# Kernel tuning notes

Measured on AMD Instinct MI355X. Metric: run time of the kernel, lower is better.

## Reference

```python
import jax, jax.numpy as jnp
import numpy as np

EPS = 1e-10

def _pairwise_cos_dist(X, Y):
    # X: (N, c), Y: (M, c) -> (N, M) cosine distance, matching torch impl exactly
    x_norm = jnp.sqrt(jnp.sum(X * X, axis=1, keepdims=True))          # (N, 1)
    y_norm = jnp.sqrt(jnp.sum(Y * Y, axis=1, keepdims=True)).T        # (1, M)
    return 1.0 - (X @ Y.T) / (x_norm + EPS) / (y_norm + EPS)

def _style_loss_cos(X, Y):
    D = _pairwise_cos_dist(X, Y)
    m1 = jnp.min(D, axis=1).mean()  # relaxed EMD, row mins
    m2 = jnp.min(D, axis=0).mean()  # col mins
    return jnp.maximum(m1, m2)

def _moment_loss(X, Y):
    # X, Y: (N, c)
    n = X.shape[0]
    mu_x = X.mean(axis=0, keepdims=True)
    mu_y = Y.mean(axis=0, keepdims=True)
    mu_d = jnp.abs(mu_x - mu_y).mean()
    Xc = X - mu_x
    Yc = Y - mu_y
    X_cov = (Xc.T @ Xc) / (n - 1)   # (c, c)
    Y_cov = (Yc.T @ Yc) / (n - 1)
    return mu_d + jnp.abs(X_cov - Y_cov).mean()

def _level_loss(X, Y):
    # X, Y: (N, c) per-batch, per-level feature sets
    return _style_loss_cos(X, Y) + _moment_loss(X, Y)

_per_batch_level_loss = jax.vmap(_level_loss)  # over leading batch dim

def _gather_points(feat, idx):
    # feat: (B, c, h, w), idx: (B, N) spatial indices -> (B, N, c)
    B, c, h, w = feat.shape
    flat = feat.reshape(B, c, h * w)
    g = jnp.take_along_axis(flat, idx[:, None, :], axis=2)  # (B, c, N)
    return jnp.swapaxes(g, 1, 2)

def _all_points(feat):
    # feat: (B, c, h, w) -> (B, h*w, c); used when h <= 32 (no subsampling)
    B, c, h, w = feat.shape
    return jnp.swapaxes(feat.reshape(B, c, h * w), 1, 2)

def setup_inputs() -> dict:
    key = jax.random.key(0)
    ks = jax.random.split(key, 11)
    shapes = [(8, 64, 256, 256), (8, 128, 128, 128), (8, 256, 64, 64), (8, 512, 32, 32)]
    inp = {}
    for i, s in enumerate(shapes):
        inp[f"target_feat{i}"] = jax.random.normal(ks[i], s, dtype=jnp.float32)
        inp[f"gen_feat{i}"] = jax.random.normal(ks[4 + i], s, dtype=jnp.float32)
    for j, hw in enumerate([256 * 256, 128 * 128, 64 * 64]):
        inp[f"idx{j}"] = jnp.sort(
            jax.random.randint(ks[8 + j], (8, 1000), 0, hw, dtype=jnp.int32), axis=1
        )
    return inp

def reference(target_feat0, target_feat1, target_feat2, target_feat3,
              gen_feat0, gen_feat1, gen_feat2, gen_feat3,
              idx0, idx1, idx2):
    B = target_feat0.shape[0]
    loss_b = jnp.zeros((B,), dtype=target_feat0.dtype)
    # levels 0-2: h > 32 -> subsample 1000 spatial points
    for t, g, idx in [(target_feat0, gen_feat0, idx0),
                      (target_feat1, gen_feat1, idx1),
                      (target_feat2, gen_feat2, idx2)]:
        loss_b = loss_b + _per_batch_level_loss(_gather_points(t, idx), _gather_points(g, idx))
    # level 3: h == 32 -> use all 1024 points
    loss_b = loss_b + _per_batch_level_loss(_all_points(target_feat3), _all_points(gen_feat3))
    return loss_b.mean()  # sum over batch / batch_size
```

## Files before the change

kernel.cpp:

```cpp
#include <hip/hip_runtime.h>
#include <cstdint>
#include <cstddef>

#define EPSC 1e-10f
typedef unsigned short u16;
typedef unsigned int u32;
typedef __attribute__((ext_vector_type(8))) short bf16x8;
typedef __attribute__((ext_vector_type(4))) float f32x4;

#define XTX_B 0u
#define XTY_B 7864320u
#define XNX_B 15728640u
#define XNY_B 23592960u
#define FB 15728640u
#define RNX_OFF (FB + 0u)
#define RNY_OFF (FB + 32768u)
#define RMIN_OFF (FB + 65536u)
#define CMIN_OFF (FB + 98304u)
#define MUX_OFF (FB + 131072u)
#define MUY_OFF (FB + 138752u)
#define COVS_OFF (FB + 146432u)
#define ACC_OFF (FB + 146464u)

struct Tabs { int c[4], N[4], mo[4]; u32 off[4]; };

__device__ __forceinline__ u16 f2bf(float f) {
  u32 u = __float_as_uint(f);
  u = (u + 0x7fffu + ((u >> 16) & 1u)) >> 16;
  return (u16)u;
}
__device__ __forceinline__ float bf2f(u16 h) { return __uint_as_float(((u32)h) << 16); }

__global__ void k_init(float* __restrict__ wsf) {
  int i = blockIdx.x * blockDim.x + threadIdx.x;
  if (i < 65536) ((unsigned*)(wsf + RMIN_OFF))[i] = 0x7f800000u;
  if (i < 33) wsf[COVS_OFF + i] = 0.f;
}

__global__ void k_gather(const float* __restrict__ tsrc, const float* __restrict__ gsrc,
                         const int* __restrict__ idx,
                         u16* __restrict__ xt, u16* __restrict__ yt,
                         u16* __restrict__ xn, u16* __restrict__ yn,
                         int c, int hw, int N) {
  __shared__ float Ls[64 * 67];
  int z = blockIdx.z, which = z >> 3, b = z & 7;
  int c0 = blockIdx.y * 64, n0 = blockIdx.x * 64;
  int tid = threadIdx.x;
  const float* src = which ? gsrc : tsrc;
  u16* dt = (which ? yt : xt) + (size_t)b * c * 1024;
  u16* dn = (which ? yn : xn) + (size_t)b * c * 1024;
  int nl = tid & 63, cb = tid >> 6;
  int n = n0 + nl;
  bool nv = n < N;
  int sp = nv ? (idx ? idx[b * N + n] : n) : 0;
  const float* sbase = src + ((size_t)b * c + c0) * hw;
#pragma unroll
  for (int r = 0; r < 16; ++r) {
    int ch = cb + r * 4;
    Ls[ch * 67 + nl] = nv ? sbase[(size_t)ch * hw + sp] : 0.f;
  }
  __syncthreads();
#pragma unroll
  for (int r = 0; r < 16; ++r) {
    int ch = cb + r * 4;
    dt[(size_t)(c0 + ch) * 1024 + n] = f2bf(Ls[ch * 67 + nl]);
  }
#pragma unroll
  for (int r = 0; r < 16; ++r) {
    int nw = cb + r * 4;
    int chw = nl;
    dn[(size_t)(n0 + nw) * c + c0 + chw] = f2bf(Ls[chw * 67 + nw]);
  }
}

__global__ void k_rnorm(const u16* __restrict__ bfb, float* __restrict__ wsf, Tabs t) {
  int L = blockIdx.z;
  int c = t.c[L];
  int zy = blockIdx.y, which = zy >> 3, b = zy & 7;
  int n = blockIdx.x * 256 + threadIdx.x;
  const u16* P = bfb + (which ? XTY_B : XTX_B) + t.off[L] + (size_t)b * c * 1024;
  float s = 0.f;
  for (int ch = 0; ch < c; ch += 4) {
#pragma unroll
    for (int u = 0; u < 4; ++u) {
      float v = bf2f(P[(size_t)(ch + u) * 1024 + n]);
      s = fmaf(v, v, s);
    }
  }
  int z = L * 8 + b;
  wsf[(which ? RNY_OFF : RNX_OFF) + (size_t)z * 1024 + n] = 1.0f / (sqrtf(s) + EPSC);
}

__global__ void k_mu(const u16* __restrict__ bfb, float* __restrict__ wsf, Tabs t) {
  int L = blockIdx.z;
  int c = t.c[L], N = t.N[L];
  int zy = blockIdx.y, which = zy >> 3, b = zy & 7;
  int wv = threadIdx.x >> 6, lane = threadIdx.x & 63;
  int ch = blockIdx.x * 4 + wv;
  if (ch >= c) return;
  const u16* P = bfb + (which ? XTY_B : XTX_B) + t.off[L] + ((size_t)b * c + ch) * 1024;
  float s = 0.f;
  for (int n = lane; n < 1024; n += 64) s += bf2f(P[n]);
#pragma unroll
  for (int off = 32; off; off >>= 1) s += __shfl_down(s, off, 64);
  if (lane == 0) wsf[(which ? MUY_OFF : MUX_OFF) + t.mo[L] + (size_t)b * c + ch] = s * (1.0f / N);
}

__global__ __launch_bounds__(256) void k_cosmin(const u16* __restrict__ bfb, float* __restrict__ wsf, Tabs t) {
  __shared__ __align__(16) u16 As[128 * 72];
  __shared__ __align__(16) u16 Bs[128 * 72];
  int z = blockIdx.z, L = z >> 3, b = z & 7;
  int c = t.c[L], N = t.N[L];
  const u16* X = bfb + XNX_B + t.off[L] + (size_t)b * c * 1024;
  const u16* Y = bfb + XNY_B + t.off[L] + (size_t)b * c * 1024;
  int i0 = blockIdx.x * 128, j0 = blockIdx.y * 128;
  int tid = threadIdx.x, lane = tid & 63, w = tid >> 6;
  int wi = w >> 1, wj = w & 1, q = lane >> 4, cl = lane & 15;
  f32x4 acc[4][4] = {};
  int srow = tid >> 3, sch = tid & 7;
  for (int k0 = 0; k0 < c; k0 += 64) {
#pragma unroll
    for (int rep = 0; rep < 4; ++rep) {
      int row = srow + rep * 32;
      uint4 va = *(const uint4*)(X + (size_t)(i0 + row) * c + k0 + sch * 8);
      uint4 vb = *(const uint4*)(Y + (size_t)(j0 + row) * c + k0 + sch * 8);
      *(uint4*)(As + row * 72 + sch * 8) = va;
      *(uint4*)(Bs + row * 72 + sch * 8) = vb;
    }
    __syncthreads();
#pragma unroll
    for (int h = 0; h < 2; ++h) {
      bf16x8 af[4], bq[4];
#pragma unroll
      for (int ti = 0; ti < 4; ++ti)
        af[ti] = *(const bf16x8*)(As + (wi * 64 + ti * 16 + cl) * 72 + h * 32 + q * 8);
#pragma unroll
      for (int tj = 0; tj < 4; ++tj)
        bq[tj] = *(const bf16x8*)(Bs + (wj * 64 + tj * 16 + cl) * 72 + h * 32 + q * 8);
#pragma unroll
      for (int ti = 0; ti < 4; ++ti)
#pragma unroll
        for (int tj = 0; tj < 4; ++tj)
          acc[ti][tj] = __builtin_amdgcn_mfma_f32_16x16x32_bf16(af[ti], bq[tj], acc[ti][tj], 0, 0, 0);
    }
    __syncthreads();
  }
  const float* rnx = wsf + RNX_OFF + (size_t)z * 1024;
  const float* rny = wsf + RNY_OFF + (size_t)z * 1024;
  unsigned* rminp = (unsigned*)(wsf + RMIN_OFF) + (size_t)z * 1024;
  unsigned* cminp = (unsigned*)(wsf + CMIN_OFF) + (size_t)z * 1024;
  const float INFV = __uint_as_float(0x7f800000u);
  int colg[4]; float rnyv[4]; float colmin[4];
#pragma unroll
  for (int tj = 0; tj < 4; ++tj) {
    colg[tj] = j0 + wj * 64 + tj * 16 + cl;
    rnyv[tj] = rny[colg[tj]];
    colmin[tj] = INFV;
  }
#pragma unroll
  for (int ti = 0; ti < 4; ++ti) {
#pragma unroll
    for (int r = 0; r < 4; ++r) {
      int rowg = i0 + wi * 64 + ti * 16 + q * 4 + r;
      float rx = rnx[rowg];
      bool rv = rowg < N;
      float rmin = INFV;
#pragma unroll
      for (int tj = 0; tj < 4; ++tj) {
        float d = 1.0f - acc[ti][tj][r] * rx * rnyv[tj];
        if (!rv || colg[tj] >= N) d = INFV;
        rmin = fminf(rmin, d);
        colmin[tj] = fminf(colmin[tj], d);
      }
      rmin = fminf(rmin, __shfl_xor(rmin, 1, 64));
      rmin = fminf(rmin, __shfl_xor(rmin, 2, 64));
      rmin = fminf(rmin, __shfl_xor(rmin, 4, 64));
      rmin = fminf(rmin, __shfl_xor(rmin, 8, 64));
      if (cl == 0 && rv) atomicMin(&rminp[rowg], __float_as_uint(rmin));
    }
  }
#pragma unroll
  for (int tj = 0; tj < 4; ++tj) {
    float cm = colmin[tj];
    cm = fminf(cm, __shfl_xor(cm, 16, 64));
    cm = fminf(cm, __shfl_xor(cm, 32, 64));
    if (q == 0 && colg[tj] < N) atomicMin(&cminp[colg[tj]], __float_as_uint(cm));
  }
}

__global__ __launch_bounds__(256) void k_cov(const u16* __restrict__ bfb, float* __restrict__ wsf, Tabs t) {
  __shared__ __align__(16) u16 SXA[128 * 40], SXB[128 * 40], SYA[128 * 40], SYB[128 * 40];
  __shared__ float wsum[4];
  int z = blockIdx.z, L = z >> 3, b = z & 7;
  int c = t.c[L], N = t.N[L];
  int ca = (c + 127) >> 7;
  if ((int)blockIdx.x >= ca || (int)blockIdx.y >= ca) return;
  int a0 = blockIdx.x * 128, b0 = blockIdx.y * 128;
  const u16* XT = bfb + XTX_B + t.off[L] + (size_t)b * c * 1024;
  const u16* YT = bfb + XTY_B + t.off[L] + (size_t)b * c * 1024;
  int tid = threadIdx.x, lane = tid & 63, w = tid >> 6;
  int wi = w >> 1, wj = w & 1, q = lane >> 4, cl = lane & 15;
  f32x4 gx[4][4] = {}, gy[4][4] = {};
  int srow = tid >> 2, sch = tid & 3;
  for (int k0 = 0; k0 < 1024; k0 += 32) {
#pragma unroll
    for (int rep = 0; rep < 2; ++rep) {
      int rr = srow + rep * 64;
      int ra = a0 + rr, rb = b0 + rr;
      uint4 zz = make_uint4(0u, 0u, 0u, 0u);
      uint4 xa = (ra < c) ? *(const uint4*)(XT + (size_t)ra * 1024 + k0 + sch * 8) : zz;
      uint4 xb = (rb < c) ? *(const uint4*)(XT + (size_t)rb * 1024 + k0 + sch * 8) : zz;
      uint4 ya = (ra < c) ? *(const uint4*)(YT + (size_t)ra * 1024 + k0 + sch * 8) : zz;
      uint4 yb = (rb < c) ? *(const uint4*)(YT + (size_t)rb * 1024 + k0 + sch * 8) : zz;
      *(uint4*)(SXA + rr * 40 + sch * 8) = xa;
      *(uint4*)(SXB + rr * 40 + sch * 8) = xb;
      *(uint4*)(SYA + rr * 40 + sch * 8) = ya;
      *(uint4*)(SYB + rr * 40 + sch * 8) = yb;
    }
    __syncthreads();
    bf16x8 af[4], bq[4];
#pragma unroll
    for (int ti = 0; ti < 4; ++ti) af[ti] = *(const bf16x8*)(SXA + (wi * 64 + ti * 16 + cl) * 40 + q * 8);
#pragma unroll
    for (int tj = 0; tj < 4; ++tj) bq[tj] = *(const bf16x8*)(SXB + (wj * 64 + tj * 16 + cl) * 40 + q * 8);
#pragma unroll
    for (int ti = 0; ti < 4; ++ti)
#pragma unroll
      for (int tj = 0; tj < 4; ++tj)
        gx[ti][tj] = __builtin_amdgcn_mfma_f32_16x16x32_bf16(af[ti], bq[tj], gx[ti][tj], 0, 0, 0);
#pragma unroll
    for (int ti = 0; ti < 4; ++ti) af[ti] = *(const bf16x8*)(SYA + (wi * 64 + ti * 16 + cl) * 40 + q * 8);
#pragma unroll
    for (int tj = 0; tj < 4; ++tj) bq[tj] = *(const bf16x8*)(SYB + (wj * 64 + tj * 16 + cl) * 40 + q * 8);
#pragma unroll
    for (int ti = 0; ti < 4; ++ti)
#pragma unroll
      for (int tj = 0; tj < 4; ++tj)
        gy[ti][tj] = __builtin_amdgcn_mfma_f32_16x16x32_bf16(af[ti], bq[tj], gy[ti][tj], 0, 0, 0);
    __syncthreads();
  }
  const float* mux = wsf + MUX_OFF + t.mo[L] + (size_t)b * c;
  const float* muy = wsf + MUY_OFF + t.mo[L] + (size_t)b * c;
  float fN = (float)N, inv1 = 1.0f / (float)(N - 1);
  float mxb[4], myb[4]; int bcol[4];
#pragma unroll
  for (int tj = 0; tj < 4; ++tj) {
    bcol[tj] = b0 + wj * 64 + tj * 16 + cl;
    bool bv = bcol[tj] < c;
    mxb[tj] = bv ? mux[bcol[tj]] : 0.f;
    myb[tj] = bv ? muy[bcol[tj]] : 0.f;
  }
  float s = 0.f;
#pragma unroll
  for (int ti = 0; ti < 4; ++ti) {
#pragma unroll
    for (int r = 0; r < 4; ++r) {
      int arow = a0 + wi * 64 + ti * 16 + q * 4 + r;
      bool av = arow < c;
      float mxa = av ? mux[arow] : 0.f;
      float mya = av ? muy[arow] : 0.f;
#pragma unroll
      for (int tj = 0; tj < 4; ++tj) {
        if (av && bcol[tj] < c) {
          float cx = (gx[ti][tj][r] - fN * mxa * mxb[tj]) * inv1;
          float cy = (gy[ti][tj][r] - fN * mya * myb[tj]) * inv1;
          s += fabsf(cx - cy);
        }
      }
    }
  }
  s += __shfl_xor(s, 1, 64);
  s += __shfl_xor(s, 2, 64);
  s += __shfl_xor(s, 4, 64);
  s += __shfl_xor(s, 8, 64);
  s += __shfl_xor(s, 16, 64);
  s += __shfl_xor(s, 32, 64);
  if (lane == 0) wsum[w] = s;
  __syncthreads();
  if (tid == 0) atomicAdd(&wsf[COVS_OFF + z], wsum[0] + wsum[1] + wsum[2] + wsum[3]);
}

__global__ void k_final(float* __restrict__ wsf, Tabs t) {
  __shared__ float red[4];
  int z = blockIdx.x, L = z >> 3, b = z & 7;
  int c = t.c[L], N = t.N[L];
  const unsigned* rmin = (const unsigned*)(wsf + RMIN_OFF) + (size_t)z * 1024;
  const unsigned* cmin = (const unsigned*)(wsf + CMIN_OFF) + (size_t)z * 1024;
  const float* mux = wsf + MUX_OFF + t.mo[L] + (size_t)b * c;
  const float* muy = wsf + MUY_OFF + t.mo[L] + (size_t)b * c;
  int tid = threadIdx.x;
  float sr = 0.f, sc = 0.f, sm = 0.f;
  for (int n = tid; n < N; n += 256) {
    sr += __uint_as_float(rmin[n]);
    sc += __uint_as_float(cmin[n]);
  }
  for (int ch = tid; ch < c; ch += 256) sm += fabsf(mux[ch] - muy[ch]);
  float vals[3] = {sr, sc, sm};
  float tot[3] = {0.f, 0.f, 0.f};
  for (int qq = 0; qq < 3; ++qq) {
    float v = vals[qq];
#pragma unroll
    for (int off = 32; off; off >>= 1) v += __shfl_down(v, off, 64);
    if ((tid & 63) == 0) red[tid >> 6] = v;
    __syncthreads();
    if (tid == 0) tot[qq] = red[0] + red[1] + red[2] + red[3];
    __syncthreads();
  }
  if (tid == 0) {
    float style = fmaxf(tot[0] / (float)N, tot[1] / (float)N);
    float mu_d = tot[2] / (float)c;
    float cov = wsf[COVS_OFF + z] / ((float)c * (float)c);
    atomicAdd(&wsf[ACC_OFF], style + mu_d + cov);
  }
}

__global__ void k_out(const float* __restrict__ wsf, float* __restrict__ out) {
  if (threadIdx.x == 0 && blockIdx.x == 0) out[0] = wsf[ACC_OFF] * 0.125f;
}

extern "C" void kernel_launch(void* const* d_in, const int* in_sizes, int n_in,
                              void* d_out, int out_size, void* d_ws, size_t ws_size,
                              hipStream_t stream) {
  (void)in_sizes; (void)n_in; (void)out_size; (void)ws_size;
  static const int LC[4] = {64, 128, 256, 512};
  static const int LN[4] = {1000, 1000, 1000, 1024};
  static const int LHW[4] = {65536, 16384, 4096, 1024};
  static const u32 LOFF[4] = {0u, 524288u, 1572864u, 3670016u};
  static const int MO[4] = {0, 512, 1536, 3584};

  float* wsf = (float*)d_ws;
  u16* bfb = (u16*)d_ws;
  Tabs t;
  for (int L = 0; L < 4; ++L) {
    t.c[L] = LC[L]; t.N[L] = LN[L]; t.mo[L] = MO[L]; t.off[L] = LOFF[L];
  }

  k_init<<<dim3(256), dim3(256), 0, stream>>>(wsf);
  for (int L = 0; L < 4; ++L) {
    const float* tf = (const float*)d_in[2 * L];
    const float* gf = (const float*)d_in[2 * L + 1];
    const int* idx = (L < 3) ? (const int*)d_in[8 + L] : nullptr;
    dim3 g(16, LC[L] / 64, 16);
    k_gather<<<g, dim3(256), 0, stream>>>(tf, gf, idx,
                                          bfb + XTX_B + LOFF[L], bfb + XTY_B + LOFF[L],
                                          bfb + XNX_B + LOFF[L], bfb + XNY_B + LOFF[L],
                                          LC[L], LHW[L], LN[L]);
  }
  k_rnorm<<<dim3(4, 16, 4), dim3(256), 0, stream>>>(bfb, wsf, t);
  k_mu<<<dim3(128, 16, 4), dim3(256), 0, stream>>>(bfb, wsf, t);
  k_cosmin<<<dim3(8, 8, 32), dim3(256), 0, stream>>>(bfb, wsf, t);
  k_cov<<<dim3(4, 4, 32), dim3(256), 0, stream>>>(bfb, wsf, t);
  k_final<<<dim3(32), dim3(256), 0, stream>>>(wsf, t);
  k_out<<<dim3(1), dim3(64), 0, stream>>>(wsf, (float*)d_out);
}
```

Baseline: 629.2 us.

## Merge gather launches and restructure covariance as symmetric per-wave tiles with fused difference

Folds the four per-level gather launches into one kernel that maps grid rows to levels. Replaces the covariance kernel with a one-wave-per-32x32-tile scheme. It covers only the upper-triangle tiles (doubling off-diagonal sums), flips the sign of Y to accumulate Gx-Gy into a single accumulator, and reads operands straight from global memory without LDS or barriers. It also remaps block IDs across XCDs for load balance. This cuts launch overhead, wasted blocks for small channel counts, and half the symmetric MFMA work, but the direct global loads may reduce operand reuse.

```diff
diff --git a/kernel.cpp b/kernel.cpp
--- a/kernel.cpp
+++ b/kernel.cpp
@@ -23,6 +23,13 @@
 #define ACC_OFF (FB + 146464u)
 
 struct Tabs { int c[4], N[4], mo[4]; u32 off[4]; };
+struct GArgs {
+  const float* t[4];
+  const float* g[4];
+  const int* idx[4];
+  int c[4], hw[4], N[4];
+  u32 off[4];
+};
 
 __device__ __forceinline__ u16 f2bf(float f) {
   u32 u = __float_as_uint(f);
@@ -37,18 +44,20 @@
   if (i < 33) wsf[COVS_OFF + i] = 0.f;
 }
 
-__global__ void k_gather(const float* __restrict__ tsrc, const float* __restrict__ gsrc,
-                         const int* __restrict__ idx,
-                         u16* __restrict__ xt, u16* __restrict__ yt,
-                         u16* __restrict__ xn, u16* __restrict__ yn,
-                         int c, int hw, int N) {
+__global__ void k_gather_all(GArgs ga, u16* __restrict__ bfb) {
   __shared__ float Ls[64 * 67];
+  int y = blockIdx.y;
+  int L = (y >= 7) ? 3 : (y >= 3) ? 2 : (y >= 1) ? 1 : 0;
+  int ybase = (L == 0) ? 0 : (L == 1) ? 1 : (L == 2) ? 3 : 7;
+  int cb64 = y - ybase;
+  int c = ga.c[L], hw = ga.hw[L], N = ga.N[L];
+  const int* idx = ga.idx[L];
   int z = blockIdx.z, which = z >> 3, b = z & 7;
-  int c0 = blockIdx.y * 64, n0 = blockIdx.x * 64;
+  int c0 = cb64 * 64, n0 = blockIdx.x * 64;
   int tid = threadIdx.x;
-  const float* src = which ? gsrc : tsrc;
-  u16* dt = (which ? yt : xt) + (size_t)b * c * 1024;
-  u16* dn = (which ? yn : xn) + (size_t)b * c * 1024;
+  const float* src = which ? ga.g[L] : ga.t[L];
+  u16* dt = bfb + (which ? XTY_B : XTX_B) + ga.off[L] + (size_t)b * c * 1024;
+  u16* dn = bfb + (which ? XNY_B : XNX_B) + ga.off[L] + (size_t)b * c * 1024;
   int nl = tid & 63, cb = tid >> 6;
   int n = n0 + nl;
   bool nv = n < N;
@@ -188,96 +197,83 @@
   }
 }
 
-__global__ __launch_bounds__(256) void k_cov(const u16* __restrict__ bfb, float* __restrict__ wsf, Tabs t) {
-  __shared__ __align__(16) u16 SXA[128 * 40], SXB[128 * 40], SYA[128 * 40], SYB[128 * 40];
-  __shared__ float wsum[4];
-  int z = blockIdx.z, L = z >> 3, b = z & 7;
+#define COVW_NBLK 370
+__global__ __launch_bounds__(256) void k_covw(const u16* __restrict__ bfb, float* __restrict__ wsf, Tabs t) {
+  int bid = blockIdx.x;
+  int qx = COVW_NBLK >> 3, rx = COVW_NBLK & 7;
+  int xcd = bid & 7, pos = bid >> 3;
+  int bsw = (xcd < rx ? xcd * (qx + 1) : rx * (qx + 1) + (xcd - rx) * qx) + pos;
+  int w = bsw * 4 + (threadIdx.x >> 6);
+  int L, b, tt, W;
+  if (w < 1088)      { int r = w;        L = 3; b = r / 136; tt = r - b * 136; W = 16; }
+  else if (w < 1376) { int r = w - 1088; L = 2; b = r / 36;  tt = r - b * 36;  W = 8; }
+  else if (w < 1456) { int r = w - 1376; L = 1; b = r / 10;  tt = r - b * 10;  W = 4; }
+  else               { int r = w - 1456; L = 0; b = r / 3;   tt = r - b * 3;   W = 2; }
+  int ti = 0, rem = tt;
+  while (rem >= W - ti) { rem -= (W - ti); ++ti; }
+  int tj = ti + rem;
   int c = t.c[L], N = t.N[L];
-  int ca = (c + 127) >> 7;
-  if ((int)blockIdx.x >= ca || (int)blockIdx.y >= ca) return;
-  int a0 = blockIdx.x * 128, b0 = blockIdx.y * 128;
-  const u16* XT = bfb + XTX_B + t.off[L] + (size_t)b * c * 1024;
-  const u16* YT = bfb + XTY_B + t.off[L] + (size_t)b * c * 1024;
-  int tid = threadIdx.x, lane = tid & 63, w = tid >> 6;
-  int wi = w >> 1, wj = w & 1, q = lane >> 4, cl = lane & 15;
-  f32x4 gx[4][4] = {}, gy[4][4] = {};
-  int srow = tid >> 2, sch = tid & 3;
+  const u16* Xp = bfb + XTX_B + t.off[L] + (size_t)b * c * 1024;
+  const u16* Yp = bfb + XTY_B + t.off[L] + (size_t)b * c * 1024;
+  int lane = threadIdx.x & 63, cl = lane & 15, qq = lane >> 4;
+  int i0 = ti * 32, j0 = tj * 32;
+  size_t aoff[2], boff[2];
+#pragma unroll
+  for (int u = 0; u < 2; ++u) {
+    aoff[u] = (size_t)(i0 + u * 16 + cl) * 1024 + qq * 8;
+    boff[u] = (size_t)(j0 + u * 16 + cl) * 1024 + qq * 8;
+  }
+  f32x4 acc[2][2] = {};
+#pragma unroll 2
   for (int k0 = 0; k0 < 1024; k0 += 32) {
-#pragma unroll
-    for (int rep = 0; rep < 2; ++rep) {
-      int rr = srow + rep * 64;
-      int ra = a0 + rr, rb = b0 + rr;
-      uint4 zz = make_uint4(0u, 0u, 0u, 0u);
-      uint4 xa = (ra < c) ? *(const uint4*)(XT + (size_t)ra * 1024 + k0 + sch * 8) : zz;
-      uint4 xb = (rb < c) ? *(const uint4*)(XT + (size_t)rb * 1024 + k0 + sch * 8) : zz;
-      uint4 ya = (ra < c) ? *(const uint4*)(YT + (size_t)ra * 1024 + k0 + sch * 8) : zz;
-      uint4 yb = (rb < c) ? *(const uint4*)(YT + (size_t)rb * 1024 + k0 + sch * 8) : zz;
-      *(uint4*)(SXA + rr * 40 + sch * 8) = xa;
-      *(uint4*)(SXB + rr * 40 + sch * 8) = xb;
-      *(uint4*)(SYA + rr * 40 + sch * 8) = ya;
-      *(uint4*)(SYB + rr * 40 + sch * 8) = yb;
-    }
-    __syncthreads();
-    bf16x8 af[4], bq[4];
-#pragma unroll
-    for (int ti = 0; ti < 4; ++ti) af[ti] = *(const bf16x8*)(SXA + (wi * 64 + ti * 16 + cl) * 40 + q * 8);
-#pragma unroll
-    for (int tj = 0; tj < 4; ++tj) bq[tj] = *(const bf16x8*)(SXB + (wj * 64 + tj * 16 + cl) * 40 + q * 8);
-#pragma unroll
-    for (int ti = 0; ti < 4; ++ti)
-#pragma unroll
-      for (int tj = 0; tj < 4; ++tj)
-        gx[ti][tj] = __builtin_amdgcn_mfma_f32_16x16x32_bf16(af[ti], bq[tj], gx[ti][tj], 0, 0, 0);
-#pragma unroll
-    for (int ti = 0; ti < 4; ++ti) af[ti] = *(const bf16x8*)(SYA + (wi * 64 + ti * 16 + cl) * 40 + q * 8);
-#pragma unroll
-    for (int tj = 0; tj < 4; ++tj) bq[tj] = *(const bf16x8*)(SYB + (wj * 64 + tj * 16 + cl) * 40 + q * 8);
-#pragma unroll
-    for (int ti = 0; ti < 4; ++ti)
-#pragma unroll
-      for (int tj = 0; tj < 4; ++tj)
-        gy[ti][tj] = __builtin_amdgcn_mfma_f32_16x16x32_bf16(af[ti], bq[tj], gy[ti][tj], 0, 0, 0);
-    __syncthreads();
+    bf16x8 ax[2], bx[2], ay[2], by[2];
+#pragma unroll
+    for (int u = 0; u < 2; ++u) {
+      ax[u] = *(const bf16x8*)(Xp + aoff[u] + k0);
+      bx[u] = *(const bf16x8*)(Xp + boff[u] + k0);
+      ay[u] = *(const bf16x8*)(Yp + aoff[u] + k0);
+      by[u] = *(const bf16x8*)(Yp + boff[u] + k0);
+    }
+#pragma unroll
+    for (int u = 0; u < 2; ++u) {
+      uint4 t4 = *(uint4*)&ay[u];
+      t4.x ^= 0x80008000u; t4.y ^= 0x80008000u; t4.z ^= 0x80008000u; t4.w ^= 0x80008000u;
+      ay[u] = *(bf16x8*)&t4;
+    }
+#pragma unroll
+    for (int u = 0; u < 2; ++u)
+#pragma unroll
+      for (int v = 0; v < 2; ++v) {
+        acc[u][v] = __builtin_amdgcn_mfma_f32_16x16x32_bf16(ax[u], bx[v], acc[u][v], 0, 0, 0);
+        acc[u][v] = __builtin_amdgcn_mfma_f32_16x16x32_bf16(ay[u], by[v], acc[u][v], 0, 0, 0);
+      }
   }
   const float* mux = wsf + MUX_OFF + t.mo[L] + (size_t)b * c;
   const float* muy = wsf + MUY_OFF + t.mo[L] + (size_t)b * c;
   float fN = (float)N, inv1 = 1.0f / (float)(N - 1);
-  float mxb[4], myb[4]; int bcol[4];
-#pragma unroll
-  for (int tj = 0; tj < 4; ++tj) {
-    bcol[tj] = b0 + wj * 64 + tj * 16 + cl;
-    bool bv = bcol[tj] < c;
-    mxb[tj] = bv ? mux[bcol[tj]] : 0.f;
-    myb[tj] = bv ? muy[bcol[tj]] : 0.f;
+  float mxj[2], myj[2];
+#pragma unroll
+  for (int v = 0; v < 2; ++v) {
+    int jg = j0 + v * 16 + cl;
+    mxj[v] = mux[jg]; myj[v] = muy[jg];
   }
   float s = 0.f;
 #pragma unroll
-  for (int ti = 0; ti < 4; ++ti) {
+  for (int u = 0; u < 2; ++u)
 #pragma unroll
     for (int r = 0; r < 4; ++r) {
-      int arow = a0 + wi * 64 + ti * 16 + q * 4 + r;
-      bool av = arow < c;
-      float mxa = av ? mux[arow] : 0.f;
-      float mya = av ? muy[arow] : 0.f;
-#pragma unroll
-      for (int tj = 0; tj < 4; ++tj) {
-        if (av && bcol[tj] < c) {
-          float cx = (gx[ti][tj][r] - fN * mxa * mxb[tj]) * inv1;
-          float cy = (gy[ti][tj][r] - fN * mya * myb[tj]) * inv1;
-          s += fabsf(cx - cy);
-        }
+      int ig = i0 + u * 16 + qq * 4 + r;
+      float mxi = mux[ig], myi = muy[ig];
+#pragma unroll
+      for (int v = 0; v < 2; ++v) {
+        float d = (acc[u][v][r] - fN * (mxi * mxj[v] - myi * myj[v])) * inv1;
+        s += fabsf(d);
       }
     }
-  }
-  s += __shfl_xor(s, 1, 64);
-  s += __shfl_xor(s, 2, 64);
-  s += __shfl_xor(s, 4, 64);
-  s += __shfl_xor(s, 8, 64);
-  s += __shfl_xor(s, 16, 64);
-  s += __shfl_xor(s, 32, 64);
-  if (lane == 0) wsum[w] = s;
-  __syncthreads();
-  if (tid == 0) atomicAdd(&wsf[COVS_OFF + z], wsum[0] + wsum[1] + wsum[2] + wsum[3]);
+  if (ti != tj) s += s;
+#pragma unroll
+  for (int o = 1; o < 64; o <<= 1) s += __shfl_xor(s, o, 64);
+  if (lane == 0) atomicAdd(&wsf[COVS_OFF + (L * 8 + b)], s);
 }
 
 __global__ void k_final(float* __restrict__ wsf, Tabs t) {
@@ -331,25 +327,21 @@
   float* wsf = (float*)d_ws;
   u16* bfb = (u16*)d_ws;
   Tabs t;
+  GArgs ga;
   for (int L = 0; L < 4; ++L) {
     t.c[L] = LC[L]; t.N[L] = LN[L]; t.mo[L] = MO[L]; t.off[L] = LOFF[L];
+    ga.t[L] = (const float*)d_in[2 * L];
+    ga.g[L] = (const float*)d_in[2 * L + 1];
+    ga.idx[L] = (L < 3) ? (const int*)d_in[8 + L] : nullptr;
+    ga.c[L] = LC[L]; ga.hw[L] = LHW[L]; ga.N[L] = LN[L]; ga.off[L] = LOFF[L];
   }
 
   k_init<<<dim3(256), dim3(256), 0, stream>>>(wsf);
-  for (int L = 0; L < 4; ++L) {
-    const float* tf = (const float*)d_in[2 * L];
-    const float* gf = (const float*)d_in[2 * L + 1];
-    const int* idx = (L < 3) ? (const int*)d_in[8 + L] : nullptr;
-    dim3 g(16, LC[L] / 64, 16);
-    k_gather<<<g, dim3(256), 0, stream>>>(tf, gf, idx,
-                                          bfb + XTX_B + LOFF[L], bfb + XTY_B + LOFF[L],
-                                          bfb + XNX_B + LOFF[L], bfb + XNY_B + LOFF[L],
-                                          LC[L], LHW[L], LN[L]);
-  }
+  k_gather_all<<<dim3(16, 15, 16), dim3(256), 0, stream>>>(ga, bfb);
   k_rnorm<<<dim3(4, 16, 4), dim3(256), 0, stream>>>(bfb, wsf, t);
   k_mu<<<dim3(128, 16, 4), dim3(256), 0, stream>>>(bfb, wsf, t);
   k_cosmin<<<dim3(8, 8, 32), dim3(256), 0, stream>>>(bfb, wsf, t);
-  k_cov<<<dim3(4, 4, 32), dim3(256), 0, stream>>>(bfb, wsf, t);
+  k_covw<<<dim3(COVW_NBLK), dim3(256), 0, stream>>>(bfb, wsf, t);
   k_final<<<dim3(32), dim3(256), 0, stream>>>(wsf, t);
   k_out<<<dim3(1), dim3(64), 0, stream>>>(wsf, (float*)d_out);
 }
```

Result: faster. 598.5 us (-4.9%).
